# Kernel tuning notes

Hardware: AMD Instinct MI355X
Metric: run time of the kernel (lower is better)

## Reference

```python
import jax, jax.numpy as jnp
import numpy as np

B, H, W, DM = 32, 32, 32, 128   # batch, height, width, d_model
DIN, N, R = 64, 16, 8           # d_inner(low_dim), d_state, dt_rank=ceil(128/16)
LN_EPS = 1e-5


def setup_inputs() -> dict:
    key = jax.random.key(0)
    ks = jax.random.split(key, 10)
    x = jax.random.normal(ks[0], (B, H, W, DM), dtype=jnp.float32)
    w_in = jax.random.normal(ks[1], (2 * DIN, DM), dtype=jnp.float32) * 0.02
    conv_w = jax.random.normal(ks[2], (DIN, 1, 3, 3), dtype=jnp.float32) * 0.1
    conv_b = jax.random.normal(ks[3], (DIN,), dtype=jnp.float32) * 0.01
    xproj_w = jax.random.normal(ks[4], (R + 2 * N, DIN), dtype=jnp.float32) * 0.05
    dtproj_w = jax.random.uniform(ks[5], (DIN, R), dtype=jnp.float32,
                                  minval=-(R ** -0.5), maxval=R ** -0.5)
    # dt bias init: inverse-softplus of dt ~ LogUniform(1e-3, 0.1)
    dt = jnp.exp(jax.random.uniform(ks[6], (DIN,)) * (np.log(0.1) - np.log(0.001)) + np.log(0.001))
    dt = jnp.clip(dt, 1e-4, None)
    dtproj_b = dt + jnp.log(-jnp.expm1(-dt))
    A_logs = jnp.log(jnp.broadcast_to(jnp.arange(1, N + 1, dtype=jnp.float32), (DIN, N)))
    Ds = jnp.ones((DIN,), dtype=jnp.float32)
    ln_g = jnp.ones((DIN,), dtype=jnp.float32)
    ln_b = jnp.zeros((DIN,), dtype=jnp.float32)
    w_out = jax.random.normal(ks[7], (DM, DIN), dtype=jnp.float32) * 0.02
    return {"x": x, "w_in": w_in, "conv_w": conv_w, "conv_b": conv_b,
            "xproj_w": xproj_w, "dtproj_w": dtproj_w, "dtproj_b": dtproj_b,
            "A_logs": A_logs, "Ds": Ds, "ln_g": ln_g, "ln_b": ln_b, "w_out": w_out}


def _silu(v):
    return v * jax.nn.sigmoid(v)


def reference(x, w_in, conv_w, conv_b, xproj_w, dtproj_w, dtproj_b,
              A_logs, Ds, ln_g, ln_b, w_out):
    b, h, w, _ = x.shape
    L = h * w
    # in_proj (no bias) and gate split
    xz = jnp.einsum('bhwc,ec->bhwe', x, w_in)           # [B,H,W,2*DIN]
    xc, z = jnp.split(xz, 2, axis=-1)
    # depthwise conv2d, SAME padding (k=3, pad=1), then SiLU
    xc = jnp.transpose(xc, (0, 3, 1, 2))                # [B,DIN,H,W]
    xc = jax.lax.conv_general_dilated(
        xc, conv_w, window_strides=(1, 1), padding=((1, 1), (1, 1)),
        feature_group_count=DIN, dimension_numbers=('NCHW', 'OIHW', 'NCHW'))
    xc = _silu(xc + conv_b[None, :, None, None])
    u = xc.reshape(b, DIN, L)                            # [B,D,L]
    # x_proj -> dt, B, C
    x_dbl = jnp.einsum('bdl,cd->bcl', u, xproj_w)        # [B,R+2N,L]
    dts, Bs, Cs = x_dbl[:, :R], x_dbl[:, R:R + N], x_dbl[:, R + N:]
    delta = jnp.einsum('brl,dr->bdl', dts, dtproj_w) + dtproj_b[None, :, None]
    delta = jax.nn.softplus(delta)                       # [B,D,L]
    A = -jnp.exp(A_logs)                                 # [D,N]
    dA = jnp.exp(delta[..., None] * A[None, :, None, :])               # [B,D,L,N]
    dBu = (delta * u)[..., None] * jnp.swapaxes(Bs, 1, 2)[:, None]     # [B,D,L,N]
    # sequential selective scan over L
    dA_s = jnp.moveaxis(dA, 2, 0)                        # [L,B,D,N]
    dBu_s = jnp.moveaxis(dBu, 2, 0)
    C_s = jnp.moveaxis(Cs, 2, 0)                         # [L,B,N]

    def step(hst, inp):
        dA_t, dBu_t, C_t = inp
        hst = dA_t * hst + dBu_t                         # [B,D,N]
        y_t = jnp.einsum('bdn,bn->bd', hst, C_t)
        return hst, y_t

    h0 = jnp.zeros((b, DIN, N), dtype=u.dtype)
    _, ys = jax.lax.scan(step, h0, (dA_s, dBu_s, C_s))   # ys: [L,B,D]
    y = jnp.moveaxis(ys, 0, 2) + Ds[None, :, None] * u   # [B,D,L]
    # back to [B,H,W,D], layernorm, gate, out_proj
    y = jnp.swapaxes(y, 1, 2).reshape(b, h, w, DIN)
    mu = jnp.mean(y, axis=-1, keepdims=True)
    var = jnp.var(y, axis=-1, keepdims=True)
    y = (y - mu) * jax.lax.rsqrt(var + LN_EPS) * ln_g + ln_b
    y = y * _silu(z)
    return jnp.einsum('bhwd,cd->bhwc', y, w_out)
```

## Files before the change

kernel.cpp:

```cpp
#include <hip/hip_runtime.h>


__global__ __launch_bounds__(256) void k1_gemm_in(
    const float* __restrict__ x, const float* __restrict__ w_in,
    float* __restrict__ xc, float* __restrict__ z)
{
    __shared__ float As[32 * 68];
    __shared__ float Ws[32 * 132];
    const int t  = threadIdx.x;
    const int p0 = blockIdx.x * 64;
    const int tx = t & 15, ty = t >> 4;

    float acc[4][8];
#pragma unroll
    for (int i = 0; i < 4; ++i)
#pragma unroll
        for (int j = 0; j < 8; ++j) acc[i][j] = 0.f;

    for (int kk = 0; kk < 128; kk += 32) {
        {
            const int m  = t >> 3;
            const int c4 = (t & 7) * 4;
            const float4 v0 = *reinterpret_cast<const float4*>(&x[(size_t)(p0 + m) * 128 + kk + c4]);
            const float4 v1 = *reinterpret_cast<const float4*>(&x[(size_t)(p0 + m + 32) * 128 + kk + c4]);
            As[(c4 + 0) * 68 + m] = v0.x; As[(c4 + 1) * 68 + m] = v0.y;
            As[(c4 + 2) * 68 + m] = v0.z; As[(c4 + 3) * 68 + m] = v0.w;
            As[(c4 + 0) * 68 + m + 32] = v1.x; As[(c4 + 1) * 68 + m + 32] = v1.y;
            As[(c4 + 2) * 68 + m + 32] = v1.z; As[(c4 + 3) * 68 + m + 32] = v1.w;
        }
        for (int i = t; i < 4096; i += 256) {
            const int c = i & 31, e = i >> 5;
            Ws[c * 132 + e] = w_in[(size_t)e * 128 + kk + c];
        }
        __syncthreads();
#pragma unroll
        for (int k = 0; k < 32; ++k) {
            const float4 a  = *reinterpret_cast<const float4*>(&As[k * 68 + (ty << 2)]);
            const float4 b0 = *reinterpret_cast<const float4*>(&Ws[k * 132 + (tx << 3)]);
            const float4 b1 = *reinterpret_cast<const float4*>(&Ws[k * 132 + (tx << 3) + 4]);
            const float am[4] = {a.x, a.y, a.z, a.w};
            const float bm[8] = {b0.x, b0.y, b0.z, b0.w, b1.x, b1.y, b1.z, b1.w};
#pragma unroll
            for (int i = 0; i < 4; ++i)
#pragma unroll
                for (int j = 0; j < 8; ++j)
                    acc[i][j] = fmaf(am[i], bm[j], acc[i][j]);
        }
        __syncthreads();
    }

    const int b  = p0 >> 10;
    const int l0 = (p0 & 1023) + (ty << 2);
    if (tx < 8) {
#pragma unroll
        for (int j = 0; j < 8; ++j) {
            const int e = (tx << 3) + j;
            *reinterpret_cast<float4*>(&xc[((size_t)b * 64 + e) * 1024 + l0]) =
                make_float4(acc[0][j], acc[1][j], acc[2][j], acc[3][j]);
        }
    } else {
        const int d0 = (tx - 8) << 3;
#pragma unroll
        for (int i = 0; i < 4; ++i) {
            const size_t p = (size_t)p0 + (ty << 2) + i;
            *reinterpret_cast<float4*>(&z[p * 64 + d0]) =
                make_float4(acc[i][0], acc[i][1], acc[i][2], acc[i][3]);
            *reinterpret_cast<float4*>(&z[p * 64 + d0 + 4]) =
                make_float4(acc[i][4], acc[i][5], acc[i][6], acc[i][7]);
        }
    }
}

__global__ __launch_bounds__(256) void k2_conv(
    const float* __restrict__ xc, const float* __restrict__ cw,
    const float* __restrict__ cb, float* __restrict__ u)
{
    __shared__ float pl[1024];
    const int bd = blockIdx.x;
    const int t  = threadIdx.x;
    const int d  = bd & 63;
    reinterpret_cast<float4*>(pl)[t] =
        reinterpret_cast<const float4*>(xc + (size_t)bd * 1024)[t];
    float w[9];
#pragma unroll
    for (int i = 0; i < 9; ++i) w[i] = cw[d * 9 + i];
    const float bias = cb[d];
    __syncthreads();
    float o[4];
#pragma unroll
    for (int i = 0; i < 4; ++i) {
        const int p  = t * 4 + i;
        const int py = p >> 5, px = p & 31;
        float s = 0.f;
#pragma unroll
        for (int ky = 0; ky < 3; ++ky) {
            const int iy = py + ky - 1;
            if (iy < 0 || iy > 31) continue;
#pragma unroll
            for (int kx = 0; kx < 3; ++kx) {
                const int ix = px + kx - 1;
                if (ix < 0 || ix > 31) continue;
                s = fmaf(pl[iy * 32 + ix], w[ky * 3 + kx], s);
            }
        }
        s += bias;
        o[i] = s / (1.f + __expf(-s));
    }
    reinterpret_cast<float4*>(u + (size_t)bd * 1024)[t] = make_float4(o[0], o[1], o[2], o[3]);
}

__global__ __launch_bounds__(256) void k3_xproj(
    const float* __restrict__ u, const float* __restrict__ xpw,
    const float* __restrict__ dtw_g, const float* __restrict__ dtb,
    float* __restrict__ delta, float* __restrict__ Bsp, float* __restrict__ Csp)
{
    __shared__ float xw[64 * 40];
    __shared__ float dw[64 * 8];
    const int t = threadIdx.x;
    for (int i = t; i < 2560; i += 256) {
        const int dd = i / 40, c = i - dd * 40;
        xw[i] = xpw[(size_t)c * 64 + dd];
    }
    for (int i = t; i < 512; i += 256) dw[i] = dtw_g[i];
    __syncthreads();

    const int gid = blockIdx.x * 256 + t;
    const int b = gid >> 10, l = gid & 1023;

    float4 acc[10];
#pragma unroll
    for (int i = 0; i < 10; ++i) acc[i] = make_float4(0.f, 0.f, 0.f, 0.f);

    const float* up = u + (size_t)b * 65536 + l;
    for (int dd = 0; dd < 64; ++dd) {
        const float uv = up[(size_t)dd * 1024];
        const float4* row = reinterpret_cast<const float4*>(&xw[dd * 40]);
#pragma unroll
        for (int i = 0; i < 10; ++i) {
            const float4 wv = row[i];
            acc[i].x = fmaf(uv, wv.x, acc[i].x);
            acc[i].y = fmaf(uv, wv.y, acc[i].y);
            acc[i].z = fmaf(uv, wv.z, acc[i].z);
            acc[i].w = fmaf(uv, wv.w, acc[i].w);
        }
    }

    float* bp = Bsp + (size_t)b * 16384 + l;
    bp[0*1024]=acc[2].x; bp[1*1024]=acc[2].y; bp[2*1024]=acc[2].z; bp[3*1024]=acc[2].w;
    bp[4*1024]=acc[3].x; bp[5*1024]=acc[3].y; bp[6*1024]=acc[3].z; bp[7*1024]=acc[3].w;
    bp[8*1024]=acc[4].x; bp[9*1024]=acc[4].y; bp[10*1024]=acc[4].z; bp[11*1024]=acc[4].w;
    bp[12*1024]=acc[5].x; bp[13*1024]=acc[5].y; bp[14*1024]=acc[5].z; bp[15*1024]=acc[5].w;
    float* cp = Csp + (size_t)b * 16384 + l;
    cp[0*1024]=acc[6].x; cp[1*1024]=acc[6].y; cp[2*1024]=acc[6].z; cp[3*1024]=acc[6].w;
    cp[4*1024]=acc[7].x; cp[5*1024]=acc[7].y; cp[6*1024]=acc[7].z; cp[7*1024]=acc[7].w;
    cp[8*1024]=acc[8].x; cp[9*1024]=acc[8].y; cp[10*1024]=acc[8].z; cp[11*1024]=acc[8].w;
    cp[12*1024]=acc[9].x; cp[13*1024]=acc[9].y; cp[14*1024]=acc[9].z; cp[15*1024]=acc[9].w;

    const float dts[8] = {acc[0].x, acc[0].y, acc[0].z, acc[0].w,
                          acc[1].x, acc[1].y, acc[1].z, acc[1].w};
    float* dp = delta + (size_t)b * 65536 + l;
    for (int dd = 0; dd < 64; ++dd) {
        const float4* r = reinterpret_cast<const float4*>(&dw[dd * 8]);
        const float4 w0 = r[0], w1 = r[1];
        float s = dtb[dd];
        s = fmaf(dts[0], w0.x, s); s = fmaf(dts[1], w0.y, s);
        s = fmaf(dts[2], w0.z, s); s = fmaf(dts[3], w0.w, s);
        s = fmaf(dts[4], w1.x, s); s = fmaf(dts[5], w1.y, s);
        s = fmaf(dts[6], w1.z, s); s = fmaf(dts[7], w1.w, s);
        const float sp = fmaxf(s, 0.f) + log1pf(__expf(-fabsf(s)));
        dp[(size_t)dd * 1024] = sp;
    }
}

__global__ __launch_bounds__(256) void k4_scan(
    const float* __restrict__ delta, const float* __restrict__ u,
    const float* __restrict__ Bsp, const float* __restrict__ Csp,
    const float* __restrict__ A_logs, const float* __restrict__ Ds,
    float* __restrict__ y)
{
    __shared__ float Ps[256][17];
    __shared__ float qs[256][17];
    __shared__ float Sp[16][17];
    __shared__ float Sq[16][17];
    const int t = threadIdx.x;
    const int pair = blockIdx.x;
    const int b = pair >> 6, d = pair & 63;

    float A[16];
#pragma unroll
    for (int n = 0; n < 16; ++n) A[n] = -__expf(A_logs[d * 16 + n]);

    const float4 d4 = *reinterpret_cast<const float4*>(delta + (size_t)pair * 1024 + t * 4);
    const float4 u4 = *reinterpret_cast<const float4*>(u     + (size_t)pair * 1024 + t * 4);
    const float du0 = d4.x * u4.x, du1 = d4.y * u4.y;
    const float du2 = d4.z * u4.z, du3 = d4.w * u4.w;

    const float* Bb = Bsp + (size_t)b * 16384 + t * 4;
    const float* Cb = Csp + (size_t)b * 16384 + t * 4;

#pragma unroll
    for (int n = 0; n < 16; ++n) {
        const float4 B4 = *reinterpret_cast<const float4*>(Bb + n * 1024);
        float a, P, q;
        a = __expf(d4.x * A[n]); P = a;   q = du0 * B4.x;
        a = __expf(d4.y * A[n]); P *= a;  q = fmaf(a, q, du1 * B4.y);
        a = __expf(d4.z * A[n]); P *= a;  q = fmaf(a, q, du2 * B4.z);
        a = __expf(d4.w * A[n]); P *= a;  q = fmaf(a, q, du3 * B4.w);
        Ps[t][n] = P; qs[t][n] = q;
    }
    __syncthreads();

    const int n = t >> 4, g = t & 15;
    float rp[16], rq[16];
    {
        float Pseg = 1.f, qseg = 0.f;
#pragma unroll
        for (int i = 0; i < 16; ++i) {
            const int c = g * 16 + i;
            rp[i] = Ps[c][n]; rq[i] = qs[c][n];
            qseg = fmaf(rp[i], qseg, rq[i]);
            Pseg *= rp[i];
        }
        Sp[g][n] = Pseg; Sq[g][n] = qseg;
    }
    __syncthreads();
    if (t < 16) {
        float h = 0.f;
#pragma unroll
        for (int s = 0; s < 16; ++s) {
            const float Pv = Sp[s][t], qv = Sq[s][t];
            Sp[s][t] = h;
            h = fmaf(Pv, h, qv);
        }
    }
    __syncthreads();
    {
        float h = Sp[g][n];
#pragma unroll
        for (int i = 0; i < 16; ++i) {
            const int c = g * 16 + i;
            qs[c][n] = h;
            h = fmaf(rp[i], h, rq[i]);
        }
    }
    __syncthreads();

    const float Dval = Ds[d];
    float y0 = Dval * u4.x, y1 = Dval * u4.y, y2 = Dval * u4.z, y3 = Dval * u4.w;
#pragma unroll
    for (int nn = 0; nn < 16; ++nn) {
        const float4 B4 = *reinterpret_cast<const float4*>(Bb + nn * 1024);
        const float4 C4 = *reinterpret_cast<const float4*>(Cb + nn * 1024);
        float h = qs[t][nn];
        float a;
        a = __expf(d4.x * A[nn]); h = fmaf(a, h, du0 * B4.x); y0 = fmaf(h, C4.x, y0);
        a = __expf(d4.y * A[nn]); h = fmaf(a, h, du1 * B4.y); y1 = fmaf(h, C4.y, y1);
        a = __expf(d4.z * A[nn]); h = fmaf(a, h, du2 * B4.z); y2 = fmaf(h, C4.z, y2);
        a = __expf(d4.w * A[nn]); h = fmaf(a, h, du3 * B4.w); y3 = fmaf(h, C4.w, y3);
    }
    *reinterpret_cast<float4*>(y + (size_t)pair * 1024 + t * 4) =
        make_float4(y0, y1, y2, y3);
}

__global__ __launch_bounds__(256) void k5_out(
    const float* __restrict__ y, const float* __restrict__ z,
    const float* __restrict__ ln_g, const float* __restrict__ ln_b,
    const float* __restrict__ w_out, float* __restrict__ out)
{
    __shared__ float yn[64 * 68];
    __shared__ float wo[64 * 132];
    const int t  = threadIdx.x;
    const int p0 = blockIdx.x * 64;
    const int b  = p0 >> 10, l0 = p0 & 1023;

    for (int i = t; i < 8192; i += 256) {
        const int c = i >> 6, dd = i & 63;
        wo[dd * 132 + c] = w_out[i];
    }

    {
        const int d = t >> 2;
        const float* yrow = y + ((size_t)b * 64 + d) * 1024 + l0;
#pragma unroll
        for (int k = 0; k < 4; ++k) {
            const int c4 = ((t & 3) + k * 4) * 4;
            const float4 v = *reinterpret_cast<const float4*>(&yrow[c4]);
            yn[(c4 + 0) * 68 + d] = v.x;
            yn[(c4 + 1) * 68 + d] = v.y;
            yn[(c4 + 2) * 68 + d] = v.z;
            yn[(c4 + 3) * 68 + d] = v.w;
        }
    }
    __syncthreads();

    const int lane = t & 63, wv = t >> 6;
    const float g = ln_g[lane], bbv = ln_b[lane];
#pragma unroll 1
    for (int i = 0; i < 16; ++i) {
        const int pl = wv * 16 + i;
        const size_t p = (size_t)p0 + pl;
        const float v  = yn[pl * 68 + lane];
        const float zv = z[p * 64 + lane];
        float s1 = v, s2 = v * v;
#pragma unroll
        for (int m = 1; m < 64; m <<= 1) {
            s1 += __shfl_xor(s1, m);
            s2 += __shfl_xor(s2, m);
        }
        const float mu   = s1 * (1.f / 64.f);
        const float var  = s2 * (1.f / 64.f) - mu * mu;
        const float rstd = rsqrtf(var + 1e-5f);
        const float sz   = zv / (1.f + __expf(-zv));
        yn[pl * 68 + lane] = ((v - mu) * rstd * g + bbv) * sz;
    }
    __syncthreads();

    const int tx = t & 31, ty = t >> 5;
    float acc[8][4];
#pragma unroll
    for (int i = 0; i < 8; ++i)
#pragma unroll
        for (int j = 0; j < 4; ++j) acc[i][j] = 0.f;

    for (int dd = 0; dd < 64; ++dd) {
        const float4 w4 = *reinterpret_cast<const float4*>(&wo[dd * 132 + (tx << 2)]);
#pragma unroll
        for (int i = 0; i < 8; ++i) {
            const float a = yn[(ty * 8 + i) * 68 + dd];
            acc[i][0] = fmaf(a, w4.x, acc[i][0]);
            acc[i][1] = fmaf(a, w4.y, acc[i][1]);
            acc[i][2] = fmaf(a, w4.z, acc[i][2]);
            acc[i][3] = fmaf(a, w4.w, acc[i][3]);
        }
    }
#pragma unroll
    for (int i = 0; i < 8; ++i) {
        const size_t p = (size_t)p0 + ty * 8 + i;
        *reinterpret_cast<float4*>(&out[p * 128 + (tx << 2)]) =
            make_float4(acc[i][0], acc[i][1], acc[i][2], acc[i][3]);
    }
}

extern "C" void kernel_launch(void* const* d_in, const int* in_sizes, int n_in,
                              void* d_out, int out_size, void* d_ws, size_t ws_size,
                              hipStream_t stream)
{
    const float* x        = (const float*)d_in[0];
    const float* w_in     = (const float*)d_in[1];
    const float* conv_w   = (const float*)d_in[2];
    const float* conv_b   = (const float*)d_in[3];
    const float* xproj_w  = (const float*)d_in[4];
    const float* dtproj_w = (const float*)d_in[5];
    const float* dtproj_b = (const float*)d_in[6];
    const float* A_logs   = (const float*)d_in[7];
    const float* Ds       = (const float*)d_in[8];
    const float* ln_g     = (const float*)d_in[9];
    const float* ln_b     = (const float*)d_in[10];
    const float* w_out    = (const float*)d_in[11];
    float* out = (float*)d_out;
    float* ws  = (float*)d_ws;

    const size_t M  = (size_t)2097152;
    float* xc    = ws;
    float* z     = ws + M;
    float* u     = ws + 2 * M;
    float* delta = ws + 3 * M;
    float* y     = ws + 4 * M;
    float* Bsp   = ws + 5 * M;
    float* Csp   = Bsp + 524288;

    k1_gemm_in<<<512, 256, 0, stream>>>(x, w_in, xc, z);
    k2_conv<<<2048, 256, 0, stream>>>(xc, conv_w, conv_b, u);
    k3_xproj<<<128, 256, 0, stream>>>(u, xproj_w, dtproj_w, dtproj_b, delta, Bsp, Csp);
    k4_scan<<<2048, 256, 0, stream>>>(delta, u, Bsp, Csp, A_logs, Ds, y);
    k5_out<<<512, 256, 0, stream>>>(y, z, ln_g, ln_b, w_out, out);
}
```

Before: 118.8 us.

## Split x_proj kernel across more blocks with shared-memory staged tiles

Restructures the x_proj/dt_proj kernel so each block handles 32 pixels instead of 256. The 40 projection outputs are spread across thread groups and the dt-projection channels across warps, with u and intermediate results staged in shared memory. This raises the block count from 128 to 1024 to fill the GPU and cuts the serial work per thread. In exchange, each block reloads the weight matrix and adds extra synchronisation.

```diff
diff --git a/kernel.cpp b/kernel.cpp
--- a/kernel.cpp
+++ b/kernel.cpp
@@ -114,61 +114,81 @@
     const float* __restrict__ dtw_g, const float* __restrict__ dtb,
     float* __restrict__ delta, float* __restrict__ Bsp, float* __restrict__ Csp)
 {
+    __shared__ float ut[64][33];
+    __shared__ float xd[40][33];
     __shared__ float xw[64 * 40];
-    __shared__ float dw[64 * 8];
-    const int t = threadIdx.x;
+    __shared__ float dwv[512];
+    const int t   = threadIdx.x;
+    const int blk = blockIdx.x;
+    const int b   = blk >> 5;
+    const int l0  = (blk & 31) * 32;
+
     for (int i = t; i < 2560; i += 256) {
         const int dd = i / 40, c = i - dd * 40;
         xw[i] = xpw[(size_t)c * 64 + dd];
     }
-    for (int i = t; i < 512; i += 256) dw[i] = dtw_g[i];
-    __syncthreads();
-
-    const int gid = blockIdx.x * 256 + t;
-    const int b = gid >> 10, l = gid & 1023;
-
-    float4 acc[10];
-#pragma unroll
-    for (int i = 0; i < 10; ++i) acc[i] = make_float4(0.f, 0.f, 0.f, 0.f);
-
-    const float* up = u + (size_t)b * 65536 + l;
-    for (int dd = 0; dd < 64; ++dd) {
-        const float uv = up[(size_t)dd * 1024];
-        const float4* row = reinterpret_cast<const float4*>(&xw[dd * 40]);
-#pragma unroll
-        for (int i = 0; i < 10; ++i) {
-            const float4 wv = row[i];
-            acc[i].x = fmaf(uv, wv.x, acc[i].x);
-            acc[i].y = fmaf(uv, wv.y, acc[i].y);
-            acc[i].z = fmaf(uv, wv.z, acc[i].z);
-            acc[i].w = fmaf(uv, wv.w, acc[i].w);
-        }
-    }
-
-    float* bp = Bsp + (size_t)b * 16384 + l;
-    bp[0*1024]=acc[2].x; bp[1*1024]=acc[2].y; bp[2*1024]=acc[2].z; bp[3*1024]=acc[2].w;
-    bp[4*1024]=acc[3].x; bp[5*1024]=acc[3].y; bp[6*1024]=acc[3].z; bp[7*1024]=acc[3].w;
-    bp[8*1024]=acc[4].x; bp[9*1024]=acc[4].y; bp[10*1024]=acc[4].z; bp[11*1024]=acc[4].w;
-    bp[12*1024]=acc[5].x; bp[13*1024]=acc[5].y; bp[14*1024]=acc[5].z; bp[15*1024]=acc[5].w;
-    float* cp = Csp + (size_t)b * 16384 + l;
-    cp[0*1024]=acc[6].x; cp[1*1024]=acc[6].y; cp[2*1024]=acc[6].z; cp[3*1024]=acc[6].w;
-    cp[4*1024]=acc[7].x; cp[5*1024]=acc[7].y; cp[6*1024]=acc[7].z; cp[7*1024]=acc[7].w;
-    cp[8*1024]=acc[8].x; cp[9*1024]=acc[8].y; cp[10*1024]=acc[8].z; cp[11*1024]=acc[8].w;
-    cp[12*1024]=acc[9].x; cp[13*1024]=acc[9].y; cp[14*1024]=acc[9].z; cp[15*1024]=acc[9].w;
-
-    const float dts[8] = {acc[0].x, acc[0].y, acc[0].z, acc[0].w,
-                          acc[1].x, acc[1].y, acc[1].z, acc[1].w};
-    float* dp = delta + (size_t)b * 65536 + l;
-    for (int dd = 0; dd < 64; ++dd) {
-        const float4* r = reinterpret_cast<const float4*>(&dw[dd * 8]);
-        const float4 w0 = r[0], w1 = r[1];
-        float s = dtb[dd];
-        s = fmaf(dts[0], w0.x, s); s = fmaf(dts[1], w0.y, s);
-        s = fmaf(dts[2], w0.z, s); s = fmaf(dts[3], w0.w, s);
-        s = fmaf(dts[4], w1.x, s); s = fmaf(dts[5], w1.y, s);
-        s = fmaf(dts[6], w1.z, s); s = fmaf(dts[7], w1.w, s);
-        const float sp = fmaxf(s, 0.f) + log1pf(__expf(-fabsf(s)));
-        dp[(size_t)dd * 1024] = sp;
+    for (int i = t; i < 512; i += 256) dwv[i] = dtw_g[i];
+
+    {
+        const int dd = t >> 2;
+        const int lq = (t & 3) * 8;
+        const float* up = u + ((size_t)b * 64 + dd) * 1024 + l0 + lq;
+        const float4 v0 = *reinterpret_cast<const float4*>(up);
+        const float4 v1 = *reinterpret_cast<const float4*>(up + 4);
+        ut[dd][lq + 0] = v0.x; ut[dd][lq + 1] = v0.y;
+        ut[dd][lq + 2] = v0.z; ut[dd][lq + 3] = v0.w;
+        ut[dd][lq + 4] = v1.x; ut[dd][lq + 5] = v1.y;
+        ut[dd][lq + 6] = v1.z; ut[dd][lq + 7] = v1.w;
+    }
+    __syncthreads();
+
+    {
+        const int pix = t & 31, cg = t >> 5;
+        const int c0 = cg * 5;
+        float a0 = 0.f, a1 = 0.f, a2 = 0.f, a3 = 0.f, a4 = 0.f;
+#pragma unroll 8
+        for (int dd = 0; dd < 64; ++dd) {
+            const float uv = ut[dd][pix];
+            const float* row = &xw[dd * 40 + c0];
+            a0 = fmaf(uv, row[0], a0);
+            a1 = fmaf(uv, row[1], a1);
+            a2 = fmaf(uv, row[2], a2);
+            a3 = fmaf(uv, row[3], a3);
+            a4 = fmaf(uv, row[4], a4);
+        }
+        xd[c0 + 0][pix] = a0; xd[c0 + 1][pix] = a1; xd[c0 + 2][pix] = a2;
+        xd[c0 + 3][pix] = a3; xd[c0 + 4][pix] = a4;
+    }
+    __syncthreads();
+
+    {
+        const int pix = t & 31, nn = t >> 5;
+        float* bp = Bsp + (size_t)b * 16384 + l0 + pix;
+        float* cp = Csp + (size_t)b * 16384 + l0 + pix;
+        bp[(size_t)nn * 1024]       = xd[8 + nn][pix];
+        bp[(size_t)(nn + 8) * 1024] = xd[16 + nn][pix];
+        cp[(size_t)nn * 1024]       = xd[24 + nn][pix];
+        cp[(size_t)(nn + 8) * 1024] = xd[32 + nn][pix];
+    }
+    {
+        const int pix = t & 31;
+        const int d0  = (t >> 5) * 8;
+        float dts[8];
+#pragma unroll
+        for (int r = 0; r < 8; ++r) dts[r] = xd[r][pix];
+        float* dp = delta + (size_t)b * 65536 + l0 + pix;
+#pragma unroll
+        for (int k = 0; k < 8; ++k) {
+            const int dd = d0 + k;
+            const float* r8 = &dwv[dd * 8];
+            float s = dtb[dd];
+            s = fmaf(dts[0], r8[0], s); s = fmaf(dts[1], r8[1], s);
+            s = fmaf(dts[2], r8[2], s); s = fmaf(dts[3], r8[3], s);
+            s = fmaf(dts[4], r8[4], s); s = fmaf(dts[5], r8[5], s);
+            s = fmaf(dts[6], r8[6], s); s = fmaf(dts[7], r8[7], s);
+            const float sp = fmaxf(s, 0.f) + log1pf(__expf(-fabsf(s)));
+            dp[(size_t)dd * 1024] = sp;
+        }
     }
 }
 
@@ -371,7 +391,7 @@
 
     k1_gemm_in<<<512, 256, 0, stream>>>(x, w_in, xc, z);
     k2_conv<<<2048, 256, 0, stream>>>(xc, conv_w, conv_b, u);
-    k3_xproj<<<128, 256, 0, stream>>>(u, xproj_w, dtproj_w, dtproj_b, delta, Bsp, Csp);
+    k3_xproj<<<1024, 256, 0, stream>>>(u, xproj_w, dtproj_w, dtproj_b, delta, Bsp, Csp);
     k4_scan<<<2048, 256, 0, stream>>>(delta, u, Bsp, Csp, A_logs, Ds, y);
     k5_out<<<512, 256, 0, stream>>>(y, z, ln_g, ln_b, w_out, out);
 }
```

Result: faster. 99.01 us (-16.6%).
